# Performance work log

Hardware: AMD Instinct MI355X
Metric: run time of the kernel (lower is better)

Reference implementation:

```python
import jax, jax.numpy as jnp
import numpy as np

EPS = 1e-6

def _phi(u):
    # positive feature map used by linear attention
    return jax.nn.elu(u) + 1.0

def setup_inputs() -> dict:
    key = jax.random.key(0)
    ks = jax.random.split(key, 5)
    B, T, D = 8, 2048, 512  # batch, seq_len, d_model == in_features == out_features
    scale = 1.0 / np.sqrt(D)
    x = jax.random.normal(ks[0], (B, T, D), dtype=jnp.float32)
    Wq = (jax.random.normal(ks[1], (D, D), dtype=jnp.float32) * scale)
    Wk = (jax.random.normal(ks[2], (D, D), dtype=jnp.float32) * scale)
    Wv = (jax.random.normal(ks[3], (D, D), dtype=jnp.float32) * scale)
    Wp = (jax.random.normal(ks[4], (D, D), dtype=jnp.float32) * scale)  # output projection (bias=False)
    return {"x": x, "Wq": Wq, "Wk": Wk, "Wv": Wv, "Wp": Wp}

def reference(x, Wq, Wk, Wv, Wp):
    # x: [B, T, D]
    B, T, D = x.shape
    q = _phi(x @ Wq)  # [B, T, D]
    k = _phi(x @ Wk)  # [B, T, D]
    v = x @ Wv        # [B, T, D]

    # recurrent linear-attention cell, stepped over time via lax.scan
    def step(carry, qkv):
        S, z = carry              # S: [B, D, D] running sum of k^T v; z: [B, D] running sum of k
        qt, kt, vt = qkv          # each [B, D]
        S = S + kt[:, :, None] * vt[:, None, :]
        z = z + kt
        num = jnp.einsum('bd,bde->be', qt, S)        # [B, D]
        den = jnp.einsum('bd,bd->b', qt, z) + EPS    # [B]
        return (S, z), num / den[:, None]

    qT = jnp.swapaxes(q, 0, 1)  # [T, B, D]
    kT = jnp.swapaxes(k, 0, 1)
    vT = jnp.swapaxes(v, 0, 1)
    init = (jnp.zeros((B, D, D), dtype=x.dtype), jnp.zeros((B, D), dtype=x.dtype))
    _, yT = jax.lax.scan(step, init, (qT, kT, vT))  # yT: [T, B, D]
    y = jnp.swapaxes(yT, 0, 1)                      # [B, T, D]
    return y @ Wp                                   # final bias-free projection
```

## Files before the change

### kernel.cpp

```cpp
#include <hip/hip_runtime.h>


typedef __attribute__((ext_vector_type(4))) float f32x4;
typedef __attribute__((ext_vector_type(8))) __bf16 bf16x8;
typedef __attribute__((ext_vector_type(8))) unsigned short ushort8;

constexpr size_t OFF_XB  = 0;
constexpr size_t OFF_WT  = OFF_XB + 16777216;
constexpr size_t OFF_Q   = OFF_WT + 2097152;
constexpr size_t OFF_KK  = OFF_Q  + 16777216;
constexpr size_t OFF_KT  = OFF_KK + 16777216;
constexpr size_t OFF_VT  = OFF_KT + 16777216;
constexpr size_t OFF_MT  = OFF_VT + 16777216;
constexpr size_t OFF_Y   = OFF_MT + 33554432;
constexpr size_t OFF_ZP  = OFF_Y  + 16777216;
constexpr size_t WS_NEED = OFF_ZP + 262144;

__device__ __forceinline__ unsigned short bfbits(float f) {
  __bf16 h = (__bf16)f;
  return __builtin_bit_cast(unsigned short, h);
}
__device__ __forceinline__ float bff(unsigned short u) {
  return (float)__builtin_bit_cast(__bf16, u);
}

__device__ __forceinline__ void gload16(const void* g, void* l) {
  __builtin_amdgcn_global_load_lds((const __attribute__((address_space(1))) void*)g,
                                   (__attribute__((address_space(3))) void*)l, 16, 0, 0);
}

__device__ __forceinline__ void stage_half(const char* gRow0, size_t ld2, int k0b,
                                           char* ldsHalf, int w, int lane) {
#pragma unroll
  for (int i = 0; i < 2; ++i) {
    int L = (w << 10) + (lane << 4) + (i << 13);
    int r = L >> 7;
    int cb = (L & 127) ^ ((r & 7) << 4);
    gload16(gRow0 + (size_t)r * ld2 + k0b + cb, ldsHalf + (w << 10) + (i << 13));
  }
}

__device__ __forceinline__ void stage_q64(const char* gRow0, size_t ld2, int k0b,
                                          char* lds, int tid) {
  int L = tid << 4;
  int r = L >> 7;
  int cb = (L & 127) ^ ((r & 7) << 4);
  gload16(gRow0 + (size_t)r * ld2 + k0b + cb, lds + L);
}

__device__ __forceinline__ const bf16x8* frag_at(const char* halfBase, int rowInHalf,
                                                 int colByte) {
  int lin = (rowInHalf << 7) + colByte;
  lin ^= (rowInHalf & 7) << 4;
  return (const bf16x8*)(halfBase + lin);
}

#define QUADH(mh, nh)                                                                  \
  _Pragma("unroll") for (int mm = 0; mm < 2; ++mm)                                     \
  _Pragma("unroll") for (int nn = 0; nn < 2; ++nn)                                     \
  _Pragma("unroll") for (int s = 0; s < 2; ++s)                                        \
      acc[(mh)*2 + mm][(nh)*2 + nn] = __builtin_amdgcn_mfma_f32_16x16x32_bf16(         \
          af[(mh)*2 + mm][s], bg[(nh)*2 + nn][s], acc[(mh)*2 + mm][(nh)*2 + nn], 0, 0, 0);

#define PHASE_TAILH(MH, NH)                                      \
  __builtin_amdgcn_s_barrier();                                  \
  asm volatile("s_waitcnt lgkmcnt(0)" ::: "memory");             \
  __builtin_amdgcn_sched_barrier(0);                             \
  __builtin_amdgcn_s_setprio(1);                                 \
  QUADH(MH, NH);                                                 \
  __builtin_amdgcn_s_setprio(0);                                 \
  __builtin_amdgcn_s_barrier();

__device__ __forceinline__ void core8h(const char* Ab, size_t lda2, const char* Bb,
                                       size_t ldb2, int nt, char* sA, char* sB,
                                       f32x4 (&acc)[4][4], int w, int lane) {
  const int wr = w >> 2, wc = w & 3;
  const int fr = lane & 15, foB = (lane >> 4) << 4;
  const int brow = (wc & 1) << 6;
  const char* gB1 = Bb + (size_t)128 * ldb2;
  bf16x8 af[4][2], bg[4][2];

  stage_half(Ab, lda2, 0, sA + 0, w, lane);
  stage_half(Bb, ldb2, 0, sB + 0, w, lane);
  stage_half(gB1, ldb2, 0, sB + 16384, w, lane);
  if (nt > 1) {
    stage_half(Ab, lda2, 128, sA + 16384, w, lane);
    asm volatile("s_waitcnt vmcnt(2)" ::: "memory");
  } else {
    asm volatile("s_waitcnt vmcnt(0)" ::: "memory");
  }
  __builtin_amdgcn_sched_barrier(0);
  __builtin_amdgcn_s_barrier();

  for (int t = 0; t < nt; ++t) {
    const int buf = t & 1;
    const char* cA = sA + buf * 16384;
    const char* cB = sB + buf * 32768 + (wc >> 1) * 16384;
    char* nA = sA + buf * 16384;
    char* nB = sB + (buf ^ 1) * 32768;
    const int kb1 = (t + 1) << 7, kb2 = (t + 2) << 7;
    const bool stB = (t + 1 < nt), stA = (t + 2 < nt);

#pragma unroll
    for (int m = 0; m < 2; ++m)
#pragma unroll
      for (int s = 0; s < 2; ++s)
        af[m][s] = *frag_at(cA, wr * 64 + m * 16 + fr, s * 64 + foB);
#pragma unroll
    for (int n = 0; n < 2; ++n)
#pragma unroll
      for (int s = 0; s < 2; ++s)
        bg[n][s] = *frag_at(cB, brow + n * 16 + fr, s * 64 + foB);
    if (stB) stage_half(Bb, ldb2, kb1, nB + 0, w, lane);
    PHASE_TAILH(0, 0)

#pragma unroll
    for (int m = 2; m < 4; ++m)
#pragma unroll
      for (int s = 0; s < 2; ++s)
        af[m][s] = *frag_at(cA, wr * 64 + m * 16 + fr, s * 64 + foB);
    if (stB) stage_half(gB1, ldb2, kb1, nB + 16384, w, lane);
    PHASE_TAILH(1, 0)

#pragma unroll
    for (int n = 2; n < 4; ++n)
#pragma unroll
      for (int s = 0; s < 2; ++s)
        bg[n][s] = *frag_at(cB, brow + n * 16 + fr, s * 64 + foB);
    if (stA) stage_half(Ab, lda2, kb2, nA, w, lane);
    PHASE_TAILH(0, 1)

    if (t < nt - 1) {
      if (stA) {
        asm volatile("s_waitcnt vmcnt(2)" ::: "memory");
      } else {
        asm volatile("s_waitcnt vmcnt(0)" ::: "memory");
      }
      __builtin_amdgcn_sched_barrier(0);
    }
    PHASE_TAILH(1, 1)
  }
}

__device__ __forceinline__ void core8h_ldsA(const char* sG, const char* Bb, size_t ldb2,
                                            int nt, char* sB, f32x4 (&acc)[4][4],
                                            int w, int lane) {
  const int wr = w >> 2, wc = w & 3;
  const int fr = lane & 15, foB = (lane >> 4) << 4;
  const int brow = (wc & 1) << 6;
  const char* gB1 = Bb + (size_t)128 * ldb2;
  bf16x8 af[4][2], bg[4][2];

  stage_half(Bb, ldb2, 0, sB + 0, w, lane);
  stage_half(gB1, ldb2, 0, sB + 16384, w, lane);
  asm volatile("s_waitcnt vmcnt(0)" ::: "memory");
  __builtin_amdgcn_sched_barrier(0);
  __builtin_amdgcn_s_barrier();

  for (int t = 0; t < nt; ++t) {
    const int buf = t & 1;
    const char* cA = sG + t * 16384;
    const char* cB = sB + buf * 32768 + (wc >> 1) * 16384;
    char* nB = sB + (buf ^ 1) * 32768;
    if (t + 1 < nt) {
      stage_half(Bb, ldb2, (t + 1) << 7, nB + 0, w, lane);
      stage_half(gB1, ldb2, (t + 1) << 7, nB + 16384, w, lane);
    }
#pragma unroll
    for (int m = 0; m < 4; ++m)
#pragma unroll
      for (int s = 0; s < 2; ++s)
        af[m][s] = *frag_at(cA, wr * 64 + m * 16 + fr, s * 64 + foB);
#pragma unroll
    for (int n = 0; n < 4; ++n)
#pragma unroll
      for (int s = 0; s < 2; ++s)
        bg[n][s] = *frag_at(cB, brow + n * 16 + fr, s * 64 + foB);
    asm volatile("s_waitcnt lgkmcnt(0)" ::: "memory");
    __builtin_amdgcn_sched_barrier(0);
    __builtin_amdgcn_s_setprio(1);
#pragma unroll
    for (int m = 0; m < 4; ++m)
#pragma unroll
      for (int n = 0; n < 4; ++n)
#pragma unroll
        for (int s = 0; s < 2; ++s)
          acc[m][n] = __builtin_amdgcn_mfma_f32_16x16x32_bf16(af[m][s], bg[n][s],
                                                              acc[m][n], 0, 0, 0);
    __builtin_amdgcn_s_setprio(0);
    if (t + 1 < nt) {
      asm volatile("s_waitcnt vmcnt(0)" ::: "memory");
      __builtin_amdgcn_sched_barrier(0);
      __builtin_amdgcn_s_barrier();
    }
  }
}

#define ACC4_INIT                                    \
  f32x4 acc[4][4];                                   \
  _Pragma("unroll") for (int m_ = 0; m_ < 4; ++m_)   \
  _Pragma("unroll") for (int n_ = 0; n_ < 4; ++n_)   \
      acc[m_][n_] = f32x4{0.f, 0.f, 0.f, 0.f};

#define ACC4_ZERO                                    \
  _Pragma("unroll") for (int m_ = 0; m_ < 4; ++m_)   \
  _Pragma("unroll") for (int n_ = 0; n_ < 4; ++n_)   \
      acc[m_][n_] = f32x4{0.f, 0.f, 0.f, 0.f};

__global__ __launch_bounds__(512, 2) void k8_qkvt(const ushort* __restrict__ xb,
                                                  const ushort* __restrict__ wt,
                                                  ushort* __restrict__ qb,
                                                  ushort* __restrict__ kkb,
                                                  ushort* __restrict__ Kt,
                                                  ushort* __restrict__ Vt,
                                                  float* __restrict__ zsumH) {
  extern __shared__ char smem[];
  const int o = blockIdx.x;
  const int wg = (o & 7) * 96 + (o >> 3);
  const int mt = wg / 6, r6 = wg % 6, z = r6 >> 1, ct = r6 & 1;
  const int tid = threadIdx.x, w = tid >> 6, lane = tid & 63;
  const ushort* wsel = wt + (z == 0 ? 0 : (z == 1 ? 262144 : 524288));
  const ushort* A = xb + (size_t)mt * 128 * 512;
  const ushort* Bp = wsel + (size_t)ct * 256 * 512;
  ACC4_INIT
  core8h((const char*)A, 1024, (const char*)Bp, 1024, 8, smem, smem + 32768, acc, w, lane);
  const int wr = w >> 2, wc = w & 3, fr = lane & 15, q4 = (lane >> 4) << 2;
  const size_t row0 = (size_t)mt * 128 + wr * 64;
  const size_t col0 = (size_t)ct * 256 + wc * 64;
  if (z == 0) {
#pragma unroll
    for (int m = 0; m < 4; ++m)
#pragma unroll
      for (int n = 0; n < 4; ++n)
#pragma unroll
        for (int r = 0; r < 4; ++r) {
          float v = acc[m][n][r];
          v = v > 0.f ? v + 1.f : __expf(v);
          qb[(row0 + m * 16 + q4 + r) * 512 + col0 + n * 16 + fr] = bfbits(v);
        }
  } else if (z == 2) {
#pragma unroll
    for (int m = 0; m < 4; ++m)
#pragma unroll
      for (int n = 0; n < 4; ++n) {
        ushort4 ov;
        ov.x = bfbits(acc[m][n][0]);
        ov.y = bfbits(acc[m][n][1]);
        ov.z = bfbits(acc[m][n][2]);
        ov.w = bfbits(acc[m][n][3]);
        *(ushort4*)&Vt[(col0 + n * 16 + fr) * 16384 + row0 + m * 16 + q4] = ov;
      }
  } else {
    float zs[4] = {0.f, 0.f, 0.f, 0.f};
#pragma unroll
    for (int m = 0; m < 4; ++m)
#pragma unroll
      for (int n = 0; n < 4; ++n) {
        float ph[4];
#pragma unroll
        for (int r = 0; r < 4; ++r) {
          float v = acc[m][n][r];
          ph[r] = v > 0.f ? v + 1.f : __expf(v);
          kkb[(row0 + m * 16 + q4 + r) * 512 + col0 + n * 16 + fr] = bfbits(ph[r]);
          zs[n] += ph[r];
        }
        ushort4 ov;
        ov.x = bfbits(ph[0]); ov.y = bfbits(ph[1]); ov.z = bfbits(ph[2]); ov.w = bfbits(ph[3]);
        *(ushort4*)&Kt[(col0 + n * 16 + fr) * 16384 + row0 + m * 16 + q4] = ov;
      }
#pragma unroll
    for (int n = 0; n < 4; ++n) {
      zs[n] += __shfl_xor(zs[n], 16, 64);
      zs[n] += __shfl_xor(zs[n], 32, 64);
    }
    float* zbuf = (float*)smem;
    if (lane < 16) {
#pragma unroll
      for (int n = 0; n < 4; ++n) zbuf[wr * 256 + wc * 64 + n * 16 + fr] = zs[n];
    }
    __syncthreads();
    if (tid < 256)
      zsumH[(size_t)mt * 512 + ct * 256 + tid] = zbuf[tid] + zbuf[256 + tid];
  }
}

__global__ __launch_bounds__(512, 2) void k8_mtst(const ushort* __restrict__ Kt,
                                                  const ushort* __restrict__ Vt,
                                                  ushort* __restrict__ Mt) {
  __shared__ __align__(16) char smem[49152];
  const int o = blockIdx.x;
  const int wg = (o & 7) * 32 + (o >> 3);
  const int et = wg >> 6, b = (wg >> 3) & 7, dt = wg & 7;
  const int tid = threadIdx.x, w = tid >> 6, lane = tid & 63;
  const int wr = w >> 2, wc = w & 3, fr = lane & 15;
  const int foB = (lane >> 4) << 4, q4 = (lane >> 4) << 2;
  const char* Ab = (const char*)(Vt + (size_t)et * 128 * 16384 + b * 2048);
  const char* Bb = (const char*)(Kt + (size_t)dt * 64 * 16384 + b * 2048);
  f32x4 acc[4];
#pragma unroll
  for (int m = 0; m < 4; ++m) acc[m] = f32x4{0.f, 0.f, 0.f, 0.f};

  stage_half(Ab, 32768, 0, smem, w, lane);
  stage_q64(Bb, 32768, 0, smem + 32768, tid);
  asm volatile("s_waitcnt vmcnt(0)" ::: "memory");
  __builtin_amdgcn_sched_barrier(0);
  __builtin_amdgcn_s_barrier();

  const int colg = dt * 64 + wc * 16 + fr;
  for (int kk = 0; kk < 32; ++kk) {
    const int c = kk >> 2, buf = kk & 1;
    if ((kk & 3) == 0) {
      ushort* Sc = Mt + (size_t)(b * 8 + c) * 262144 + colg;
#pragma unroll
      for (int m = 0; m < 4; ++m)
#pragma unroll
        for (int r = 0; r < 4; ++r)
          Sc[(size_t)(et * 128 + wr * 64 + m * 16 + q4 + r) * 512] = bfbits(acc[m][r]);
      (void)c;
    }
    if (kk + 1 < 32) {
      const int k0b = ((kk + 1) >> 2) * 512 + ((kk + 1) & 3) * 128;
      stage_half(Ab, 32768, k0b, smem + ((buf ^ 1) << 14), w, lane);
      stage_q64(Bb, 32768, k0b, smem + 32768 + ((buf ^ 1) << 13), tid);
    }
    const char* cA = smem + (buf << 14);
    const char* cB = smem + 32768 + (buf << 13);
    bf16x8 af[4][2], bg[2];
#pragma unroll
    for (int m = 0; m < 4; ++m)
#pragma unroll
      for (int s = 0; s < 2; ++s)
        af[m][s] = *frag_at(cA, wr * 64 + m * 16 + fr, s * 64 + foB);
#pragma unroll
    for (int s = 0; s < 2; ++s) bg[s] = *frag_at(cB, wc * 16 + fr, s * 64 + foB);
    asm volatile("s_waitcnt lgkmcnt(0)" ::: "memory");
    __builtin_amdgcn_sched_barrier(0);
    __builtin_amdgcn_s_setprio(1);
#pragma unroll
    for (int m = 0; m < 4; ++m)
#pragma unroll
      for (int s = 0; s < 2; ++s)
        acc[m] = __builtin_amdgcn_mfma_f32_16x16x32_bf16(af[m][s], bg[s], acc[m], 0, 0, 0);
    __builtin_amdgcn_s_setprio(0);
    asm volatile("s_waitcnt vmcnt(0)" ::: "memory");
    __builtin_amdgcn_sched_barrier(0);
    __builtin_amdgcn_s_barrier();
  }
}

__global__ __launch_bounds__(512, 2) void k8_y(const ushort* __restrict__ qb,
                                               const ushort* __restrict__ kkb,
                                               const ushort* __restrict__ St,
                                               const ushort* __restrict__ Vt,
                                               const float* __restrict__ zsumH,
                                               ushort* __restrict__ Y) {
  extern __shared__ char smem[];
  const int o = blockIdx.x;
  const int wg = (o & 7) * 32 + (o >> 3);
  const int bc = wg >> 2, rh = (wg >> 1) & 1, ch = wg & 1;
  const int b = bc >> 3, c = bc & 7;
  const int tid = threadIdx.x, w = tid >> 6, lane = tid & 63;
  const int wr = w >> 2, wc = w & 3, fr = lane & 15, q4 = (lane >> 4) << 2;
  char* sA = smem + 65536;
  char* sB = smem + 98304;
  const char* qptr = (const char*)(qb + (size_t)bc * 131072 + (size_t)rh * 65536);

  ACC4_INIT
  core8h(qptr, 1024, (const char*)(kkb + (size_t)bc * 131072), 1024, 8, sA, sB, acc, w, lane);

  float rs[4][4];
#pragma unroll
  for (int m = 0; m < 4; ++m)
#pragma unroll
    for (int r = 0; r < 4; ++r) rs[m][r] = 0.f;
#pragma unroll
  for (int m = 0; m < 4; ++m)
#pragma unroll
    for (int n = 0; n < 4; ++n)
#pragma unroll
      for (int r = 0; r < 4; ++r) {
        int rowL = wr * 64 + m * 16 + q4 + r;
        int col = wc * 64 + n * 16 + fr;
        float v = (col <= rh * 128 + rowL) ? acc[m][n][r] : 0.f;
        rs[m][r] += v;
        int byte = (rowL << 7) + ((col & 63) << 1);
        byte ^= (rowL & 7) << 4;
        *(__bf16*)(smem + (wc << 14) + byte) = (__bf16)v;
      }
#pragma unroll
  for (int m = 0; m < 4; ++m)
#pragma unroll
    for (int r = 0; r < 4; ++r) {
      rs[m][r] += __shfl_xor(rs[m][r], 1, 64);
      rs[m][r] += __shfl_xor(rs[m][r], 2, 64);
      rs[m][r] += __shfl_xor(rs[m][r], 4, 64);
      rs[m][r] += __shfl_xor(rs[m][r], 8, 64);
    }
  float* red = (float*)sA;
  float* zpl = red + 512;
  float* dend = zpl + 512;
  if (fr == 0) {
#pragma unroll
    for (int m = 0; m < 4; ++m)
#pragma unroll
      for (int r = 0; r < 4; ++r) red[wc * 128 + wr * 64 + m * 16 + q4 + r] = rs[m][r];
  }
  {
    float a = 0.f;
    for (int cp = 0; cp < c; ++cp)
      a += zsumH[(size_t)((b * 8 + cp) * 2) * 512 + tid] +
           zsumH[(size_t)((b * 8 + cp) * 2 + 1) * 512 + tid];
    zpl[tid] = a;
  }
  __syncthreads();
  {
    int rl = tid >> 2, quarter = tid & 3;
    int trow = bc * 256 + rh * 128 + rl;
    const ushort* qrow = qb + (size_t)trow * 512 + quarter * 128;
    const float* zq = zpl + quarter * 128;
    float s = 0.f;
    for (int j = 0; j < 128; j += 8) {
      ushort8 qv = *(const ushort8*)&qrow[j];
#pragma unroll
      for (int u = 0; u < 8; ++u) s = fmaf(bff(qv[u]), zq[j + u], s);
    }
    s += __shfl_xor(s, 1, 64);
    s += __shfl_xor(s, 2, 64);
    if (quarter == 0)
      dend[rl] = s + red[rl] + red[128 + rl] + red[256 + rl] + red[384 + rl] + 1e-6f;
  }
  __syncthreads();
  float dinv[4][4];
#pragma unroll
  for (int m = 0; m < 4; ++m)
#pragma unroll
    for (int r = 0; r < 4; ++r) dinv[m][r] = 1.f / dend[wr * 64 + m * 16 + q4 + r];
  __syncthreads();

  ACC4_ZERO
  core8h(qptr, 1024, (const char*)(St + (size_t)bc * 262144 + (size_t)ch * 131072), 1024, 8,
         sA, sB, acc, w, lane);
  core8h_ldsA(smem, (const char*)(Vt + (size_t)ch * 256 * 16384 + (size_t)bc * 256), 32768,
              rh ? 4 : 2, sB, acc, w, lane);

#pragma unroll
  for (int m = 0; m < 4; ++m)
#pragma unroll
    for (int n = 0; n < 4; ++n)
#pragma unroll
      for (int r = 0; r < 4; ++r) {
        size_t row = (size_t)bc * 256 + rh * 128 + wr * 64 + m * 16 + q4 + r;
        size_t col = (size_t)ch * 256 + wc * 64 + n * 16 + fr;
        Y[row * 512 + col] = bfbits(acc[m][n][r] * dinv[m][r]);
      }
}

__global__ __launch_bounds__(512, 2) void k8_out(const ushort* __restrict__ Y,
                                                 const ushort* __restrict__ wt,
                                                 float* __restrict__ out) {
  extern __shared__ char smem[];
  const int o = blockIdx.x;
  const int wg = (o & 7) * 32 + (o >> 3);
  const int mt = wg >> 1, ct = wg & 1;
  const int tid = threadIdx.x, w = tid >> 6, lane = tid & 63;
  ACC4_INIT
  core8h((const char*)(Y + (size_t)mt * 65536), 1024,
         (const char*)(wt + 786432 + (size_t)ct * 131072), 1024, 8,
         smem, smem + 32768, acc, w, lane);
  const int wr = w >> 2, wc = w & 3, fr = lane & 15, q4 = (lane >> 4) << 2;
  const size_t row0 = (size_t)mt * 128 + wr * 64;
  const size_t col0 = (size_t)ct * 256 + wc * 64;
#pragma unroll
  for (int m = 0; m < 4; ++m)
#pragma unroll
    for (int n = 0; n < 4; ++n)
#pragma unroll
      for (int r = 0; r < 4; ++r)
        out[(row0 + m * 16 + q4 + r) * 512 + col0 + n * 16 + fr] = acc[m][n][r];
}

__global__ __launch_bounds__(256) void k_pre(const float* __restrict__ x,
                                             const float* __restrict__ Wq,
                                             const float* __restrict__ Wk,
                                             const float* __restrict__ Wv,
                                             const float* __restrict__ Wp,
                                             ushort* __restrict__ xb,
                                             ushort* __restrict__ wt) {
  __shared__ float tile[64][65];
  if (blockIdx.x < 4096) {
    size_t i = ((size_t)blockIdx.x * 256 + threadIdx.x) * 8;
    float4 f0 = *(const float4*)&x[i], f1 = *(const float4*)&x[i + 4];
    ushort8 ov;
    ov[0] = bfbits(f0.x); ov[1] = bfbits(f0.y); ov[2] = bfbits(f0.z); ov[3] = bfbits(f0.w);
    ov[4] = bfbits(f1.x); ov[5] = bfbits(f1.y); ov[6] = bfbits(f1.z); ov[7] = bfbits(f1.w);
    *(ushort8*)&xb[i] = ov;
  } else {
    const int g = blockIdx.x - 4096;
    const int bz = g >> 6, rem = g & 63, bxw = rem >> 3, byw = rem & 7;
    const float* src = bz == 0 ? Wq : bz == 1 ? Wk : bz == 2 ? Wv : Wp;
    ushort* dst = wt + (size_t)bz * 262144;
    const int d0 = bxw * 64, n0 = byw * 64;
    const int tr = threadIdx.x >> 4, tc = (threadIdx.x & 15) << 2;
#pragma unroll
    for (int it = 0; it < 4; ++it) {
      float4 f = *(const float4*)&src[(size_t)(d0 + it * 16 + tr) * 512 + n0 + tc];
      tile[it * 16 + tr][tc + 0] = f.x;
      tile[it * 16 + tr][tc + 1] = f.y;
      tile[it * 16 + tr][tc + 2] = f.z;
      tile[it * 16 + tr][tc + 3] = f.w;
    }
    __syncthreads();
#pragma unroll
    for (int it = 0; it < 4; ++it) {
      int n = it * 16 + tr;
      ushort4 ov;
      ov.x = bfbits(tile[tc + 0][n]);
      ov.y = bfbits(tile[tc + 1][n]);
      ov.z = bfbits(tile[tc + 2][n]);
      ov.w = bfbits(tile[tc + 3][n]);
      *(ushort4*)&dst[(size_t)(n0 + n) * 512 + d0 + tc] = ov;
    }
  }
}

extern "C" void kernel_launch(void* const* d_in, const int* in_sizes, int n_in,
                              void* d_out, int out_size, void* d_ws, size_t ws_size,
                              hipStream_t stream) {
  const float* x  = (const float*)d_in[0];
  const float* Wq = (const float*)d_in[1];
  const float* Wk = (const float*)d_in[2];
  const float* Wv = (const float*)d_in[3];
  const float* Wp = (const float*)d_in[4];
  float* out = (float*)d_out;
  char* ws8 = (char*)d_ws;
  if (ws_size < WS_NEED) return;

  ushort* xb  = (ushort*)(ws8 + OFF_XB);
  ushort* wt  = (ushort*)(ws8 + OFF_WT);
  ushort* qb  = (ushort*)(ws8 + OFF_Q);
  ushort* kkb = (ushort*)(ws8 + OFF_KK);
  ushort* Kt  = (ushort*)(ws8 + OFF_KT);
  ushort* Vt  = (ushort*)(ws8 + OFF_VT);
  ushort* Mt  = (ushort*)(ws8 + OFF_MT);
  ushort* Y   = (ushort*)(ws8 + OFF_Y);
  float*  zpH = (float*)(ws8 + OFF_ZP);

  constexpr int SMEM_H = 98304, SMEM_Y = 163840;
  hipFuncSetAttribute((const void*)k8_qkvt, hipFuncAttributeMaxDynamicSharedMemorySize, SMEM_H);
  hipFuncSetAttribute((const void*)k8_y,    hipFuncAttributeMaxDynamicSharedMemorySize, SMEM_Y);
  hipFuncSetAttribute((const void*)k8_out,  hipFuncAttributeMaxDynamicSharedMemorySize, SMEM_H);

  k_pre<<<4352, 256, 0, stream>>>(x, Wq, Wk, Wv, Wp, xb, wt);
  k8_qkvt<<<768, 512, SMEM_H, stream>>>(xb, wt, qb, kkb, Kt, Vt, zpH);
  k8_mtst<<<256, 512, 0, stream>>>(Kt, Vt, Mt);
  k8_y<<<256, 512, SMEM_Y, stream>>>(qb, kkb, Mt, Vt, zpH, Y);
  k8_out<<<256, 512, SMEM_H, stream>>>(Y, wt, out);
}
```

Measured before the change: 135.1 us.

## Switch QKV and output GEMMs to 128x128 tiles with 4-wave blocks

Result: slower. 141.0 us (+4.4%).

```diff
diff --git a/kernel.cpp b/kernel.cpp
--- a/kernel.cpp
+++ b/kernel.cpp
@@ -29,6 +29,67 @@
                                    (__attribute__((address_space(3))) void*)l, 16, 0, 0);
 }
 
+
+__device__ __forceinline__ void stage32(const char* g, size_t ld2, int k0b, char* lds,
+                                        int tid) {
+#pragma unroll
+  for (int i = 0; i < 2; ++i) {
+    int L = (tid << 4) + (i << 12);
+    int r = L >> 6;
+    int cb = (L & 63) ^ ((r & 3) << 4);
+    gload16(g + (size_t)r * ld2 + k0b + cb, lds + L);
+  }
+}
+
+__device__ __forceinline__ const bf16x8* frag32(const char* base, int row, int kchunkB) {
+  int lin = (row << 6) + kchunkB;
+  lin ^= (row & 3) << 4;
+  return (const bf16x8*)(base + lin);
+}
+
+__device__ __forceinline__ void core128(const char* Ab, size_t lda2, const char* Bb,
+                                        size_t ldb2, int nt, char* sA, char* sB,
+                                        f32x4 (&acc)[4][4], int w, int lane) {
+  const int wr = w >> 1, wc = w & 1;
+  const int fr = lane & 15, kB = (lane >> 4) << 4;
+  const int tid = (w << 6) + lane;
+
+  stage32(Ab, lda2, 0, sA, tid);
+  stage32(Bb, ldb2, 0, sB, tid);
+  asm volatile("s_waitcnt vmcnt(0)" ::: "memory");
+  __builtin_amdgcn_sched_barrier(0);
+  __builtin_amdgcn_s_barrier();
+
+  for (int t = 0; t < nt; ++t) {
+    const int buf = t & 1;
+    if (t + 1 < nt) {
+      stage32(Ab, lda2, (t + 1) << 6, sA + ((buf ^ 1) << 13), tid);
+      stage32(Bb, ldb2, (t + 1) << 6, sB + ((buf ^ 1) << 13), tid);
+    }
+    const char* cA = sA + (buf << 13);
+    const char* cB = sB + (buf << 13);
+    bf16x8 af[4], bg[4];
+#pragma unroll
+    for (int m = 0; m < 4; ++m) af[m] = *frag32(cA, wr * 64 + m * 16 + fr, kB);
+#pragma unroll
+    for (int n = 0; n < 4; ++n) bg[n] = *frag32(cB, wc * 64 + n * 16 + fr, kB);
+    asm volatile("s_waitcnt lgkmcnt(0)" ::: "memory");
+    __builtin_amdgcn_sched_barrier(0);
+    __builtin_amdgcn_s_setprio(1);
+#pragma unroll
+    for (int m = 0; m < 4; ++m)
+#pragma unroll
+      for (int n = 0; n < 4; ++n)
+        acc[m][n] = __builtin_amdgcn_mfma_f32_16x16x32_bf16(af[m], bg[n], acc[m][n], 0, 0, 0);
+    __builtin_amdgcn_s_setprio(0);
+    if (t + 1 < nt) {
+      asm volatile("s_waitcnt vmcnt(0)" ::: "memory");
+    }
+    __builtin_amdgcn_sched_barrier(0);
+    __builtin_amdgcn_s_barrier();
+  }
+}
+
 __device__ __forceinline__ void stage_half(const char* gRow0, size_t ld2, int k0b,
                                            char* ldsHalf, int w, int lane) {
 #pragma unroll
@@ -207,26 +268,26 @@
   _Pragma("unroll") for (int n_ = 0; n_ < 4; ++n_)   \
       acc[m_][n_] = f32x4{0.f, 0.f, 0.f, 0.f};
 
-__global__ __launch_bounds__(512, 2) void k8_qkvt(const ushort* __restrict__ xb,
+__global__ __launch_bounds__(256, 4) void k8_qkvt(const ushort* __restrict__ xb,
                                                   const ushort* __restrict__ wt,
                                                   ushort* __restrict__ qb,
                                                   ushort* __restrict__ kkb,
                                                   ushort* __restrict__ Kt,
                                                   ushort* __restrict__ Vt,
                                                   float* __restrict__ zsumH) {
-  extern __shared__ char smem[];
+  __shared__ __align__(16) char smem[32768];
   const int o = blockIdx.x;
-  const int wg = (o & 7) * 96 + (o >> 3);
-  const int mt = wg / 6, r6 = wg % 6, z = r6 >> 1, ct = r6 & 1;
+  const int wg = (o & 7) * 192 + (o >> 3);
+  const int mt = wg / 12, rem = wg % 12, z = rem >> 2, ct = rem & 3;
   const int tid = threadIdx.x, w = tid >> 6, lane = tid & 63;
   const ushort* wsel = wt + (z == 0 ? 0 : (z == 1 ? 262144 : 524288));
-  const ushort* A = xb + (size_t)mt * 128 * 512;
-  const ushort* Bp = wsel + (size_t)ct * 256 * 512;
   ACC4_INIT
-  core8h((const char*)A, 1024, (const char*)Bp, 1024, 8, smem, smem + 32768, acc, w, lane);
-  const int wr = w >> 2, wc = w & 3, fr = lane & 15, q4 = (lane >> 4) << 2;
+  core128((const char*)(xb + (size_t)mt * 128 * 512), 1024,
+          (const char*)(wsel + (size_t)ct * 128 * 512), 1024, 16,
+          smem, smem + 16384, acc, w, lane);
+  const int wr = w >> 1, wc = w & 1, fr = lane & 15, q4 = (lane >> 4) << 2;
   const size_t row0 = (size_t)mt * 128 + wr * 64;
-  const size_t col0 = (size_t)ct * 256 + wc * 64;
+  const size_t col0 = (size_t)ct * 128 + wc * 64;
   if (z == 0) {
 #pragma unroll
     for (int m = 0; m < 4; ++m)
@@ -276,11 +337,11 @@
     float* zbuf = (float*)smem;
     if (lane < 16) {
 #pragma unroll
-      for (int n = 0; n < 4; ++n) zbuf[wr * 256 + wc * 64 + n * 16 + fr] = zs[n];
+      for (int n = 0; n < 4; ++n) zbuf[wr * 128 + wc * 64 + n * 16 + fr] = zs[n];
     }
     __syncthreads();
-    if (tid < 256)
-      zsumH[(size_t)mt * 512 + ct * 256 + tid] = zbuf[tid] + zbuf[256 + tid];
+    if (tid < 128)
+      zsumH[(size_t)mt * 512 + ct * 128 + tid] = zbuf[tid] + zbuf[128 + tid];
   }
 }
 
@@ -316,7 +377,6 @@
 #pragma unroll
         for (int r = 0; r < 4; ++r)
           Sc[(size_t)(et * 128 + wr * 64 + m * 16 + q4 + r) * 512] = bfbits(acc[m][r]);
-      (void)c;
     }
     if (kk + 1 < 32) {
       const int k0b = ((kk + 1) >> 2) * 512 + ((kk + 1) & 3) * 128;
@@ -455,21 +515,21 @@
       }
 }
 
-__global__ __launch_bounds__(512, 2) void k8_out(const ushort* __restrict__ Y,
+__global__ __launch_bounds__(256, 4) void k8_out(const ushort* __restrict__ Y,
                                                  const ushort* __restrict__ wt,
                                                  float* __restrict__ out) {
-  extern __shared__ char smem[];
+  __shared__ __align__(16) char smem[32768];
   const int o = blockIdx.x;
-  const int wg = (o & 7) * 32 + (o >> 3);
-  const int mt = wg >> 1, ct = wg & 1;
+  const int wg = (o & 7) * 64 + (o >> 3);
+  const int mt = wg >> 2, ct = wg & 3;
   const int tid = threadIdx.x, w = tid >> 6, lane = tid & 63;
   ACC4_INIT
-  core8h((const char*)(Y + (size_t)mt * 65536), 1024,
-         (const char*)(wt + 786432 + (size_t)ct * 131072), 1024, 8,
-         smem, smem + 32768, acc, w, lane);
-  const int wr = w >> 2, wc = w & 3, fr = lane & 15, q4 = (lane >> 4) << 2;
+  core128((const char*)(Y + (size_t)mt * 65536), 1024,
+          (const char*)(wt + 786432 + (size_t)ct * 65536), 1024, 16,
+          smem, smem + 16384, acc, w, lane);
+  const int wr = w >> 1, wc = w & 1, fr = lane & 15, q4 = (lane >> 4) << 2;
   const size_t row0 = (size_t)mt * 128 + wr * 64;
-  const size_t col0 = (size_t)ct * 256 + wc * 64;
+  const size_t col0 = (size_t)ct * 128 + wc * 64;
 #pragma unroll
   for (int m = 0; m < 4; ++m)
 #pragma unroll
@@ -545,14 +605,12 @@
   ushort* Y   = (ushort*)(ws8 + OFF_Y);
   float*  zpH = (float*)(ws8 + OFF_ZP);
 
-  constexpr int SMEM_H = 98304, SMEM_Y = 163840;
-  hipFuncSetAttribute((const void*)k8_qkvt, hipFuncAttributeMaxDynamicSharedMemorySize, SMEM_H);
-  hipFuncSetAttribute((const void*)k8_y,    hipFuncAttributeMaxDynamicSharedMemorySize, SMEM_Y);
-  hipFuncSetAttribute((const void*)k8_out,  hipFuncAttributeMaxDynamicSharedMemorySize, SMEM_H);
+  constexpr int SMEM_Y = 163840;
+  hipFuncSetAttribute((const void*)k8_y, hipFuncAttributeMaxDynamicSharedMemorySize, SMEM_Y);
 
   k_pre<<<4352, 256, 0, stream>>>(x, Wq, Wk, Wv, Wp, xb, wt);
-  k8_qkvt<<<768, 512, SMEM_H, stream>>>(xb, wt, qb, kkb, Kt, Vt, zpH);
+  k8_qkvt<<<1536, 256, 0, stream>>>(xb, wt, qb, kkb, Kt, Vt, zpH);
   k8_mtst<<<256, 512, 0, stream>>>(Kt, Vt, Mt);
   k8_y<<<256, 512, SMEM_Y, stream>>>(qb, kkb, Mt, Vt, zpH, Y);
-  k8_out<<<256, 512, SMEM_H, stream>>>(Y, wt, out);
-}
+  k8_out<<<512, 256, 0, stream>>>(Y, wt, out);
+}
```

## Fuse Q/K/V projections into one block sharing the staged x tile

Applied to the files above, without the earlier changes.

Result: faster. 129.2 us (-4.4%).

```diff
diff --git a/kernel.cpp b/kernel.cpp
--- a/kernel.cpp
+++ b/kernel.cpp
@@ -216,72 +216,135 @@
                                                   float* __restrict__ zsumH) {
   extern __shared__ char smem[];
   const int o = blockIdx.x;
-  const int wg = (o & 7) * 96 + (o >> 3);
-  const int mt = wg / 6, r6 = wg % 6, z = r6 >> 1, ct = r6 & 1;
+  const int wg = (o & 7) * 64 + (o >> 3);
+  const int mt = wg >> 2, ct = wg & 3;
   const int tid = threadIdx.x, w = tid >> 6, lane = tid & 63;
-  const ushort* wsel = wt + (z == 0 ? 0 : (z == 1 ? 262144 : 524288));
-  const ushort* A = xb + (size_t)mt * 128 * 512;
-  const ushort* Bp = wsel + (size_t)ct * 256 * 512;
-  ACC4_INIT
-  core8h((const char*)A, 1024, (const char*)Bp, 1024, 8, smem, smem + 32768, acc, w, lane);
-  const int wr = w >> 2, wc = w & 3, fr = lane & 15, q4 = (lane >> 4) << 2;
+  const int wr = w >> 2, wc = w & 3;
+  const int fr = lane & 15, foB = (lane >> 4) << 4, q4 = (lane >> 4) << 2;
+  const char* Ab = (const char*)(xb + (size_t)mt * 128 * 512);
+  const char* Bz[3];
+  Bz[0] = (const char*)(wt + (size_t)ct * 65536);
+  Bz[1] = (const char*)(wt + 262144 + (size_t)ct * 65536);
+  Bz[2] = (const char*)(wt + 524288 + (size_t)ct * 65536);
+  char* sA = smem;
+  char* sB0 = smem + 32768;
+  char* sB1 = smem + 65536;
+  char* sB2 = smem + 98304;
+
+  f32x4 acc[3][4][2];
+#pragma unroll
+  for (int z = 0; z < 3; ++z)
+#pragma unroll
+    for (int m = 0; m < 4; ++m)
+#pragma unroll
+      for (int n = 0; n < 2; ++n) acc[z][m][n] = f32x4{0.f, 0.f, 0.f, 0.f};
+
+  stage_half(Ab, 1024, 0, sA, w, lane);
+  stage_half(Bz[0], 1024, 0, sB0, w, lane);
+  stage_half(Bz[1], 1024, 0, sB1, w, lane);
+  stage_half(Bz[2], 1024, 0, sB2, w, lane);
+  asm volatile("s_waitcnt vmcnt(0)" ::: "memory");
+  __builtin_amdgcn_sched_barrier(0);
+  __builtin_amdgcn_s_barrier();
+
+  for (int t = 0; t < 8; ++t) {
+    const int buf = t & 1;
+    const int bo = buf << 14, nbo = (buf ^ 1) << 14;
+    if (t + 1 < 8) {
+      const int kb = (t + 1) << 7;
+      stage_half(Ab, 1024, kb, sA + nbo, w, lane);
+      stage_half(Bz[0], 1024, kb, sB0 + nbo, w, lane);
+      stage_half(Bz[1], 1024, kb, sB1 + nbo, w, lane);
+      stage_half(Bz[2], 1024, kb, sB2 + nbo, w, lane);
+    }
+    bf16x8 af[4][2], bg[3][2][2];
+#pragma unroll
+    for (int m = 0; m < 4; ++m)
+#pragma unroll
+      for (int s = 0; s < 2; ++s)
+        af[m][s] = *frag_at(sA + bo, wr * 64 + m * 16 + fr, s * 64 + foB);
+#pragma unroll
+    for (int n = 0; n < 2; ++n)
+#pragma unroll
+      for (int s = 0; s < 2; ++s) {
+        bg[0][n][s] = *frag_at(sB0 + bo, wc * 32 + n * 16 + fr, s * 64 + foB);
+        bg[1][n][s] = *frag_at(sB1 + bo, wc * 32 + n * 16 + fr, s * 64 + foB);
+        bg[2][n][s] = *frag_at(sB2 + bo, wc * 32 + n * 16 + fr, s * 64 + foB);
+      }
+    asm volatile("s_waitcnt lgkmcnt(0)" ::: "memory");
+    __builtin_amdgcn_sched_barrier(0);
+    __builtin_amdgcn_s_setprio(1);
+#pragma unroll
+    for (int z = 0; z < 3; ++z)
+#pragma unroll
+      for (int m = 0; m < 4; ++m)
+#pragma unroll
+        for (int n = 0; n < 2; ++n)
+#pragma unroll
+          for (int s = 0; s < 2; ++s)
+            acc[z][m][n] = __builtin_amdgcn_mfma_f32_16x16x32_bf16(af[m][s], bg[z][n][s],
+                                                                   acc[z][m][n], 0, 0, 0);
+    __builtin_amdgcn_s_setprio(0);
+    if (t + 1 < 8) {
+      asm volatile("s_waitcnt vmcnt(0)" ::: "memory");
+    }
+    __builtin_amdgcn_sched_barrier(0);
+    __builtin_amdgcn_s_barrier();
+  }
+
   const size_t row0 = (size_t)mt * 128 + wr * 64;
-  const size_t col0 = (size_t)ct * 256 + wc * 64;
-  if (z == 0) {
-#pragma unroll
-    for (int m = 0; m < 4; ++m)
-#pragma unroll
-      for (int n = 0; n < 4; ++n)
-#pragma unroll
-        for (int r = 0; r < 4; ++r) {
-          float v = acc[m][n][r];
-          v = v > 0.f ? v + 1.f : __expf(v);
-          qb[(row0 + m * 16 + q4 + r) * 512 + col0 + n * 16 + fr] = bfbits(v);
-        }
-  } else if (z == 2) {
-#pragma unroll
-    for (int m = 0; m < 4; ++m)
-#pragma unroll
-      for (int n = 0; n < 4; ++n) {
-        ushort4 ov;
-        ov.x = bfbits(acc[m][n][0]);
-        ov.y = bfbits(acc[m][n][1]);
-        ov.z = bfbits(acc[m][n][2]);
-        ov.w = bfbits(acc[m][n][3]);
-        *(ushort4*)&Vt[(col0 + n * 16 + fr) * 16384 + row0 + m * 16 + q4] = ov;
+  const size_t col0 = (size_t)ct * 128 + wc * 32;
+#pragma unroll
+  for (int m = 0; m < 4; ++m)
+#pragma unroll
+    for (int n = 0; n < 2; ++n)
+#pragma unroll
+      for (int r = 0; r < 4; ++r) {
+        float v = acc[0][m][n][r];
+        v = v > 0.f ? v + 1.f : __expf(v);
+        qb[(row0 + m * 16 + q4 + r) * 512 + col0 + n * 16 + fr] = bfbits(v);
       }
-  } else {
-    float zs[4] = {0.f, 0.f, 0.f, 0.f};
-#pragma unroll
-    for (int m = 0; m < 4; ++m)
-#pragma unroll
-      for (int n = 0; n < 4; ++n) {
-        float ph[4];
-#pragma unroll
-        for (int r = 0; r < 4; ++r) {
-          float v = acc[m][n][r];
-          ph[r] = v > 0.f ? v + 1.f : __expf(v);
-          kkb[(row0 + m * 16 + q4 + r) * 512 + col0 + n * 16 + fr] = bfbits(ph[r]);
-          zs[n] += ph[r];
-        }
-        ushort4 ov;
-        ov.x = bfbits(ph[0]); ov.y = bfbits(ph[1]); ov.z = bfbits(ph[2]); ov.w = bfbits(ph[3]);
-        *(ushort4*)&Kt[(col0 + n * 16 + fr) * 16384 + row0 + m * 16 + q4] = ov;
+#pragma unroll
+  for (int m = 0; m < 4; ++m)
+#pragma unroll
+    for (int n = 0; n < 2; ++n) {
+      ushort4 ov;
+      ov.x = bfbits(acc[2][m][n][0]);
+      ov.y = bfbits(acc[2][m][n][1]);
+      ov.z = bfbits(acc[2][m][n][2]);
+      ov.w = bfbits(acc[2][m][n][3]);
+      *(ushort4*)&Vt[(col0 + n * 16 + fr) * 16384 + row0 + m * 16 + q4] = ov;
+    }
+  float zs[2] = {0.f, 0.f};
+#pragma unroll
+  for (int m = 0; m < 4; ++m)
+#pragma unroll
+    for (int n = 0; n < 2; ++n) {
+      float ph[4];
+#pragma unroll
+      for (int r = 0; r < 4; ++r) {
+        float v = acc[1][m][n][r];
+        ph[r] = v > 0.f ? v + 1.f : __expf(v);
+        kkb[(row0 + m * 16 + q4 + r) * 512 + col0 + n * 16 + fr] = bfbits(ph[r]);
+        zs[n] += ph[r];
       }
-#pragma unroll
-    for (int n = 0; n < 4; ++n) {
-      zs[n] += __shfl_xor(zs[n], 16, 64);
-      zs[n] += __shfl_xor(zs[n], 32, 64);
-    }
-    float* zbuf = (float*)smem;
-    if (lane < 16) {
-#pragma unroll
-      for (int n = 0; n < 4; ++n) zbuf[wr * 256 + wc * 64 + n * 16 + fr] = zs[n];
-    }
-    __syncthreads();
-    if (tid < 256)
-      zsumH[(size_t)mt * 512 + ct * 256 + tid] = zbuf[tid] + zbuf[256 + tid];
-  }
+      ushort4 ov;
+      ov.x = bfbits(ph[0]); ov.y = bfbits(ph[1]); ov.z = bfbits(ph[2]); ov.w = bfbits(ph[3]);
+      *(ushort4*)&Kt[(col0 + n * 16 + fr) * 16384 + row0 + m * 16 + q4] = ov;
+    }
+#pragma unroll
+  for (int n = 0; n < 2; ++n) {
+    zs[n] += __shfl_xor(zs[n], 16, 64);
+    zs[n] += __shfl_xor(zs[n], 32, 64);
+  }
+  float* zbuf = (float*)smem;
+  if (lane < 16) {
+#pragma unroll
+    for (int n = 0; n < 2; ++n) zbuf[wr * 128 + wc * 32 + n * 16 + fr] = zs[n];
+  }
+  __syncthreads();
+  if (tid < 128)
+    zsumH[(size_t)mt * 512 + ct * 128 + tid] = zbuf[tid] + zbuf[128 + tid];
 }
 
 __global__ __launch_bounds__(512, 2) void k8_mtst(const ushort* __restrict__ Kt,
@@ -316,7 +379,6 @@
 #pragma unroll
         for (int r = 0; r < 4; ++r)
           Sc[(size_t)(et * 128 + wr * 64 + m * 16 + q4 + r) * 512] = bfbits(acc[m][r]);
-      (void)c;
     }
     if (kk + 1 < 32) {
       const int k0b = ((kk + 1) >> 2) * 512 + ((kk + 1) & 3) * 128;
@@ -545,13 +607,13 @@
   ushort* Y   = (ushort*)(ws8 + OFF_Y);
   float*  zpH = (float*)(ws8 + OFF_ZP);
 
-  constexpr int SMEM_H = 98304, SMEM_Y = 163840;
-  hipFuncSetAttribute((const void*)k8_qkvt, hipFuncAttributeMaxDynamicSharedMemorySize, SMEM_H);
+  constexpr int SMEM_QKVT = 131072, SMEM_H = 98304, SMEM_Y = 163840;
+  hipFuncSetAttribute((const void*)k8_qkvt, hipFuncAttributeMaxDynamicSharedMemorySize, SMEM_QKVT);
   hipFuncSetAttribute((const void*)k8_y,    hipFuncAttributeMaxDynamicSharedMemorySize, SMEM_Y);
   hipFuncSetAttribute((const void*)k8_out,  hipFuncAttributeMaxDynamicSharedMemorySize, SMEM_H);
 
   k_pre<<<4352, 256, 0, stream>>>(x, Wq, Wk, Wv, Wp, xb, wt);
-  k8_qkvt<<<768, 512, SMEM_H, stream>>>(xb, wt, qb, kkb, Kt, Vt, zpH);
+  k8_qkvt<<<512, 512, SMEM_QKVT, stream>>>(xb, wt, qb, kkb, Kt, Vt, zpH);
   k8_mtst<<<256, 512, 0, stream>>>(Kt, Vt, Mt);
   k8_y<<<256, 512, SMEM_Y, stream>>>(qb, kkb, Mt, Vt, zpH, Y);
   k8_out<<<256, 512, SMEM_H, stream>>>(Y, wt, out);
```
